# Optimization experiments

Hardware: AMD Instinct MI355X
Metric: run time of the kernel (lower is better)

Reference implementation:

```python
import jax, jax.numpy as jnp
import numpy as np

B, N, D, H = 2, 4096, 512, 8
HD = D // H

def setup_inputs() -> dict:
    key = jax.random.key(0)
    ks = jax.random.split(key, 5)
    s = 1.0 / np.sqrt(D)
    return {
        "x": jax.random.normal(ks[0], (B, N, D), dtype=jnp.float32),
        "W_qkv": jax.random.uniform(ks[1], (D, 3 * D), minval=-s, maxval=s, dtype=jnp.float32),
        "b_qkv": jax.random.uniform(ks[2], (3 * D,), minval=-s, maxval=s, dtype=jnp.float32),
        "W_out": jax.random.uniform(ks[3], (D, D), minval=-s, maxval=s, dtype=jnp.float32),
        "b_out": jax.random.uniform(ks[4], (D,), minval=-s, maxval=s, dtype=jnp.float32),
    }

def reference(x, W_qkv, b_qkv, W_out, b_out):
    Bq, Nq, Dq = x.shape
    scale = HD ** -0.5
    qkv = x @ W_qkv + b_qkv                      # [B,N,3D]
    qkv = qkv.reshape(Bq, Nq, 3, H, HD)
    q, k, v = (jnp.moveaxis(qkv[:, :, i], 2, 1) for i in range(3))  # [B,H,N,hd]
    attn = jnp.einsum('bhqd,bhkd->bhqk', q, k) * scale   # [B,H,N,N]
    causal = jnp.tril(jnp.ones((Nq, Nq), dtype=bool))
    attn = jnp.where(causal, attn, -jnp.inf)
    attn = jax.nn.softmax(attn, axis=-1)
    out = jnp.einsum('bhqk,bhkd->bhqd', attn, v)         # [B,H,N,hd]
    out = jnp.moveaxis(out, 1, 2).reshape(Bq, Nq, Dq)
    return out @ W_out + b_out
```

## Files before the change

kernel.cpp:

```cpp
#include <hip/hip_runtime.h>
#include <hip/hip_bf16.h>


typedef __bf16 bf16_t;
typedef __bf16 bf16x4 __attribute__((ext_vector_type(4)));
typedef __bf16 bf16x8 __attribute__((ext_vector_type(8)));
typedef float  f32x4  __attribute__((ext_vector_type(4)));


__global__ void convert_f32_bf16(const float* __restrict__ in, bf16_t* __restrict__ out) {
    int i = blockIdx.x * 256 + threadIdx.x;
    float4 v = ((const float4*)in)[i];
    bf16x4 o;
    o[0] = (bf16_t)v.x; o[1] = (bf16_t)v.y; o[2] = (bf16_t)v.z; o[3] = (bf16_t)v.w;
    ((bf16x4*)out)[i] = o;
}

__global__ void transpose_tiled(const float* __restrict__ in, bf16_t* __restrict__ out, int N) {
    __shared__ bf16_t T[64][72];
    const int tid = threadIdx.x;
    const int n0 = blockIdx.x * 64, k0 = blockIdx.y * 64;
    #pragma unroll
    for (int pass = 0; pass < 4; ++pass) {
        int kk = pass * 16 + (tid >> 4), nn = (tid & 15) * 4;
        float4 v = *(const float4*)(in + (size_t)(k0 + kk) * N + n0 + nn);
        T[nn + 0][kk] = (bf16_t)v.x; T[nn + 1][kk] = (bf16_t)v.y;
        T[nn + 2][kk] = (bf16_t)v.z; T[nn + 3][kk] = (bf16_t)v.w;
    }
    __syncthreads();
    #pragma unroll
    for (int pass = 0; pass < 2; ++pass) {
        int n = pass * 32 + (tid >> 3), c8 = (tid & 7) * 8;
        *(bf16x8*)(out + (size_t)(n0 + n) * 512 + k0 + c8) = *(const bf16x8*)&T[n][c8];
    }
}


template <int MODE, int TN>
__global__ __launch_bounds__(256) void gemm_bt(
    const bf16_t* __restrict__ A, const bf16_t* __restrict__ Bt,
    const float* __restrict__ bias,
    bf16_t* __restrict__ Qg, bf16_t* __restrict__ Kg, bf16_t* __restrict__ Vt,
    float* __restrict__ Cout)
{
    constexpr int NI = (TN == 128) ? 4 : 2;
    __shared__ bf16_t As[128][72];
    __shared__ bf16_t Bs[TN][72];
    const int tid  = threadIdx.x;
    const int wid  = tid >> 6, lane = tid & 63, l16 = lane & 15, quad = lane >> 4;
    const int wr   = (TN == 128) ? (wid >> 1) * 64 : wid * 32;
    const int wc   = (TN == 128) ? (wid & 1) * 64 : 0;
    const int m0   = blockIdx.y * 128, n0 = blockIdx.x * TN;

    f32x4 acc[NI][4] = {};

    for (int kk = 0; kk < 512; kk += 64) {
        __syncthreads();
        #pragma unroll
        for (int i = 0; i < 4; ++i) {
            int c = tid + i * 256, row = c >> 3, col8 = (c & 7) * 8;
            *(uint4*)&As[row][col8] = *(const uint4*)(A + (size_t)(m0 + row) * 512 + kk + col8);
        }
        #pragma unroll
        for (int i = 0; i < TN / 32; ++i) {
            int c = tid + i * 256, row = c >> 3, col8 = (c & 7) * 8;
            *(uint4*)&Bs[row][col8] = *(const uint4*)(Bt + (size_t)(n0 + row) * 512 + kk + col8);
        }
        __syncthreads();
        #pragma unroll
        for (int s = 0; s < 2; ++s) {
            bf16x8 a[NI], b[4];
            #pragma unroll
            for (int i = 0; i < NI; ++i) a[i] = *(const bf16x8*)&As[wr + i * 16 + l16][s * 32 + quad * 8];
            #pragma unroll
            for (int j = 0; j < 4; ++j) b[j] = *(const bf16x8*)&Bs[wc + j * 16 + l16][s * 32 + quad * 8];
            #pragma unroll
            for (int i = 0; i < NI; ++i)
                #pragma unroll
                for (int j = 0; j < 4; ++j)
                    acc[i][j] = __builtin_amdgcn_mfma_f32_16x16x32_bf16(a[i], b[j], acc[i][j], 0, 0, 0);
        }
    }

    const float qscale = 0.18033688011112042f;
    #pragma unroll
    for (int i = 0; i < NI; ++i) {
        int mrow = m0 + wr + i * 16 + quad * 4;
        #pragma unroll
        for (int j = 0; j < 4; ++j) {
            int cgl = n0 + wc + j * 16 + l16;
            float bv = bias[cgl];
            #pragma unroll
            for (int r = 0; r < 4; ++r) {
                int m = mrow + r;
                float val = acc[i][j][r] + bv;
                if (MODE == 0) {
                    int which = cgl >> 9, hh = (cgl >> 6) & 7, hd = cgl & 63;
                    int b_ = m >> 12, n = m & 4095, bh = b_ * 8 + hh;
                    if (which == 0)      Qg[((size_t)bh * 4096 + n) * 64 + hd] = (bf16_t)(val * qscale);
                    else if (which == 1) Kg[((size_t)bh * 4096 + n) * 64 + hd] = (bf16_t)val;
                    else                 Vt[((size_t)bh * 64 + hd) * 4096 + n] = (bf16_t)val;
                } else {
                    Cout[(size_t)m * 512 + cgl] = val;
                }
            }
        }
    }
}


__global__ __launch_bounds__(256, 3) void attn_ns2(
    const bf16_t* __restrict__ Qg, const bf16_t* __restrict__ Kg,
    const bf16_t* __restrict__ Vt,
    float* __restrict__ o_part, float* __restrict__ l_part, int nsplit)
{
    __shared__ bf16_t Ks[2][64][72];
    __shared__ bf16_t Vs[2][64][72];
    __shared__ bf16_t Ps[4][16][72];

    const int tid  = threadIdx.x;
    const int w    = tid >> 6, lane = tid & 63, l16 = lane & 15, quad = lane >> 4;
    const int bh   = blockIdx.x & 15, pr = (blockIdx.x >> 4) & 15, h = blockIdx.x >> 8;

    float* ob = o_part + (size_t)(h * 16 + bh) * 4096 * 64;
    float* lb = l_part + (size_t)(h * 16 + bh) * 4096;

    const int srow = tid >> 3, scol = (tid & 7) * 8;
    const int srow1 = srow + 32;
    const float MSHIFT = 12.0f;

    bf16x8 ones;
    #pragma unroll
    for (int j = 0; j < 8; ++j) ones[j] = (bf16_t)1.0f;

    uint4 kr0, kr1, vr0, vr1;

    for (int ph = 0; ph < 2; ++ph) {
        const int st = ph ? (31 - pr) : pr;
        const int T  = 2 * st + 2;
        const int b0 = (h * T) / nsplit, b1 = ((h + 1) * T) / nsplit;

        int qrow[2];
        bf16x8 qf[2][2];
        #pragma unroll
        for (int s = 0; s < 2; ++s) {
            qrow[s] = st * 128 + s * 64 + w * 16 + l16;
            const bf16_t* qp = Qg + ((size_t)bh * 4096 + qrow[s]) * 64;
            qf[s][0] = *(const bf16x8*)(qp + quad * 8);
            qf[s][1] = *(const bf16x8*)(qp + 32 + quad * 8);
        }

        f32x4 o[2][4] = {};
        f32x4 lacc[2] = {};

        {
            const size_t kb = ((size_t)bh * 4096 + b0 * 64) * 64;
            const size_t vb = (size_t)bh * 64 * 4096 + b0 * 64;
            kr0 = *(const uint4*)(Kg + kb + (size_t)srow * 64 + scol);
            kr1 = *(const uint4*)(Kg + kb + (size_t)srow1 * 64 + scol);
            vr0 = *(const uint4*)(Vt + vb + (size_t)srow * 4096 + scol);
            vr1 = *(const uint4*)(Vt + vb + (size_t)srow1 * 4096 + scol);
        }
        __syncthreads();

        for (int kt = b0; kt < b1; ++kt) {
            const int cur = kt & 1;
            *(uint4*)&Ks[cur][srow][scol]  = kr0;
            *(uint4*)&Ks[cur][srow1][scol] = kr1;
            *(uint4*)&Vs[cur][srow][scol]  = vr0;
            *(uint4*)&Vs[cur][srow1][scol] = vr1;
            __syncthreads();

            if (kt + 1 < b1) {
                const size_t kb = ((size_t)bh * 4096 + (kt + 1) * 64) * 64;
                const size_t vb = (size_t)bh * 64 * 4096 + (kt + 1) * 64;
                kr0 = *(const uint4*)(Kg + kb + (size_t)srow * 64 + scol);
                kr1 = *(const uint4*)(Kg + kb + (size_t)srow1 * 64 + scol);
                vr0 = *(const uint4*)(Vt + vb + (size_t)srow * 4096 + scol);
                vr1 = *(const uint4*)(Vt + vb + (size_t)srow1 * 4096 + scol);
            }

            bf16x8 kf[4][2], vf[4][2];
            #pragma unroll
            for (int cb = 0; cb < 4; ++cb) {
                kf[cb][0] = *(const bf16x8*)&Ks[cur][cb * 16 + l16][quad * 8];
                kf[cb][1] = *(const bf16x8*)&Ks[cur][cb * 16 + l16][32 + quad * 8];
            }
            #pragma unroll
            for (int j = 0; j < 4; ++j) {
                vf[j][0] = *(const bf16x8*)&Vs[cur][j * 16 + l16][quad * 8];
                vf[j][1] = *(const bf16x8*)&Vs[cur][j * 16 + l16][32 + quad * 8];
            }

            #pragma unroll
            for (int s = 0; s < 2; ++s) {
                const int diag = 2 * st + s;
                if (kt > diag) continue;

                f32x4 sv[4] = {};
                #pragma unroll
                for (int cb = 0; cb < 4; ++cb) {
                    sv[cb] = __builtin_amdgcn_mfma_f32_16x16x32_bf16(kf[cb][0], qf[s][0], sv[cb], 0, 0, 0);
                    sv[cb] = __builtin_amdgcn_mfma_f32_16x16x32_bf16(kf[cb][1], qf[s][1], sv[cb], 0, 0, 0);
                }

                if (kt == diag) {
                    #pragma unroll
                    for (int cb = 0; cb < 4; ++cb) {
                        const int keyg = kt * 64 + cb * 16 + quad * 4;
                        #pragma unroll
                        for (int r = 0; r < 4; ++r)
                            if (keyg + r > qrow[s]) sv[cb][r] = -1e30f;
                    }
                }

                #pragma unroll
                for (int cb = 0; cb < 4; ++cb) {
                    bf16x4 pk;
                    #pragma unroll
                    for (int r = 0; r < 4; ++r)
                        pk[r] = (bf16_t)__builtin_amdgcn_exp2f(sv[cb][r] - MSHIFT);
                    *(bf16x4*)&Ps[w][l16][cb * 16 + quad * 4] = pk;
                }
                bf16x8 pa0 = *(const bf16x8*)&Ps[w][l16][quad * 8];
                bf16x8 pa1 = *(const bf16x8*)&Ps[w][l16][32 + quad * 8];

                #pragma unroll
                for (int j = 0; j < 4; ++j) {
                    o[s][j] = __builtin_amdgcn_mfma_f32_16x16x32_bf16(pa0, vf[j][0], o[s][j], 0, 0, 0);
                    o[s][j] = __builtin_amdgcn_mfma_f32_16x16x32_bf16(pa1, vf[j][1], o[s][j], 0, 0, 0);
                }
                lacc[s] = __builtin_amdgcn_mfma_f32_16x16x32_bf16(pa0, ones, lacc[s], 0, 0, 0);
                lacc[s] = __builtin_amdgcn_mfma_f32_16x16x32_bf16(pa1, ones, lacc[s], 0, 0, 0);
            }
        }

        #pragma unroll
        for (int s = 0; s < 2; ++s)
            #pragma unroll
            for (int r = 0; r < 4; ++r) {
                int n = st * 128 + s * 64 + w * 16 + quad * 4 + r;
                #pragma unroll
                for (int j = 0; j < 4; ++j)
                    ob[(size_t)n * 64 + j * 16 + l16] = o[s][j][r];
                if (l16 == 0) lb[n] = lacc[s][r];
            }
    }
}

__global__ void combine_kernel(const float* __restrict__ o_part,
                               const float* __restrict__ l_part,
                               bf16_t* __restrict__ Og, int ns)
{
    int t = blockIdx.x * 256 + threadIdx.x;
    int oct = t & 7, n = (t >> 3) & 4095, bh = t >> 15;
    size_t base = ((size_t)bh * 4096 + n) * 64 + oct * 8;
    f32x4 s0 = {}, s1 = {};
    float l = 0.f;
    for (int h = 0; h < ns; ++h) {
        const float* op = o_part + (size_t)h * 16 * 4096 * 64 + base;
        s0 += *(const f32x4*)op;
        s1 += *(const f32x4*)(op + 4);
        l  += l_part[(size_t)h * 16 * 4096 + (size_t)bh * 4096 + n];
    }
    float inv = 1.0f / l;
    bf16x8 res;
    #pragma unroll
    for (int j = 0; j < 4; ++j) {
        res[j]     = (bf16_t)(s0[j] * inv);
        res[j + 4] = (bf16_t)(s1[j] * inv);
    }
    *(bf16x8*)(Og + ((size_t)((bh >> 3) * 4096 + n)) * 512 + (bh & 7) * 64 + oct * 8) = res;
}


extern "C" void kernel_launch(void* const* d_in, const int* in_sizes, int n_in,
                              void* d_out, int out_size, void* d_ws, size_t ws_size,
                              hipStream_t stream) {
    const float* x    = (const float*)d_in[0];
    const float* Wqkv = (const float*)d_in[1];
    const float* bqkv = (const float*)d_in[2];
    const float* Wout = (const float*)d_in[3];
    const float* bout = (const float*)d_in[4];
    float* out = (float*)d_out;

    char* ws = (char*)d_ws;
    bf16_t* xb  = (bf16_t*)(ws);
    bf16_t* WqT = (bf16_t*)(ws + 8388608);
    bf16_t* WoT = (bf16_t*)(ws + 9961472);
    bf16_t* Qg  = (bf16_t*)(ws + 10485760);
    bf16_t* Kg  = (bf16_t*)(ws + 18874368);
    bf16_t* Vt  = (bf16_t*)(ws + 27262976);

    const int nsplit = (ws_size >= 86769664ULL) ? 3 : 2;
    float* o_part = (float*)(ws + 35651584);
    float* l_part = (float*)(ws + 35651584 + (size_t)nsplit * 16777216);

    convert_f32_bf16<<<4096, 256, 0, stream>>>(x, xb);
    transpose_tiled<<<dim3(24, 8), 256, 0, stream>>>(Wqkv, WqT, 1536);
    transpose_tiled<<<dim3(8, 8), 256, 0, stream>>>(Wout, WoT, 512);

    gemm_bt<0, 128><<<dim3(12, 64), 256, 0, stream>>>(xb, WqT, bqkv, Qg, Kg, Vt, nullptr);

    attn_ns2<<<256 * nsplit, 256, 0, stream>>>(Qg, Kg, Vt, o_part, l_part, nsplit);
    combine_kernel<<<2048, 256, 0, stream>>>(o_part, l_part, xb , nsplit);

    gemm_bt<1, 64><<<dim3(8, 64), 256, 0, stream>>>(xb, WoT, bout, nullptr, nullptr, nullptr, out);
}
```

Baseline: 200.7 us.

## Load GEMM tiles directly to LDS with XOR swizzle; split V transpose out

The GEMM tile loads now go through global_load_lds (16-byte direct-to-LDS), and an XOR-swizzled unpadded layout replaces the padded LDS arrays to avoid bank conflicts without register staging. The QKV epilogue previously wrote V transposed with strided scattered stores. It now writes V row-major into a scratch region that aliases o_part, and a separate swizzled LDS transpose kernel produces Vt. This adds one kernel launch and an extra pass over V in exchange for coalesced epilogue stores and cheaper GEMM loads.

```diff
diff --git a/kernel.cpp b/kernel.cpp
--- a/kernel.cpp
+++ b/kernel.cpp
@@ -6,6 +6,12 @@
 typedef __bf16 bf16x4 __attribute__((ext_vector_type(4)));
 typedef __bf16 bf16x8 __attribute__((ext_vector_type(8)));
 typedef float  f32x4  __attribute__((ext_vector_type(4)));
+
+__device__ __forceinline__ void gload_lds16(const bf16_t* g, bf16_t* l) {
+    __builtin_amdgcn_global_load_lds(
+        (const __attribute__((address_space(1))) void*)g,
+        (__attribute__((address_space(3))) void*)l, 16, 0, 0);
+}
 
 
 __global__ void convert_f32_bf16(const float* __restrict__ in, bf16_t* __restrict__ out) {
@@ -35,19 +41,44 @@
     }
 }
 
+__global__ void transpose_v(const bf16_t* __restrict__ Vg, bf16_t* __restrict__ Vt) {
+    __shared__ bf16_t T[64 * 64];
+    const int tid = threadIdx.x;
+    const int bh = blockIdx.x >> 6, n0 = (blockIdx.x & 63) * 64;
+    const bf16_t* src = Vg + ((size_t)bh * 4096 + n0) * 64;
+    #pragma unroll
+    for (int i = 0; i < 2; ++i) {
+        int c = tid + i * 256, n = c >> 3, h8 = (c & 7) * 8;
+        bf16x8 v = *(const bf16x8*)(src + (size_t)n * 64 + h8);
+        const int swz = (n >> 3) ^ (h8 >> 3);
+        bf16_t* base = &T[swz * 8 + (n & 7)];
+        #pragma unroll
+        for (int j = 0; j < 8; ++j) base[(h8 + j) * 64] = v[j];
+    }
+    __syncthreads();
+    bf16_t* dst = Vt + (size_t)bh * 64 * 4096 + n0;
+    #pragma unroll
+    for (int i = 0; i < 2; ++i) {
+        int c = tid + i * 256, hd = c >> 3, cn = c & 7;
+        *(bf16x8*)(dst + (size_t)hd * 4096 + cn * 8) =
+            *(const bf16x8*)&T[hd * 64 + ((cn ^ (hd >> 3)) * 8)];
+    }
+}
+
 
 template <int MODE, int TN>
 __global__ __launch_bounds__(256) void gemm_bt(
     const bf16_t* __restrict__ A, const bf16_t* __restrict__ Bt,
     const float* __restrict__ bias,
-    bf16_t* __restrict__ Qg, bf16_t* __restrict__ Kg, bf16_t* __restrict__ Vt,
+    bf16_t* __restrict__ Qg, bf16_t* __restrict__ Kg, bf16_t* __restrict__ Vg,
     float* __restrict__ Cout)
 {
     constexpr int NI = (TN == 128) ? 4 : 2;
-    __shared__ bf16_t As[128][72];
-    __shared__ bf16_t Bs[TN][72];
+    __shared__ bf16_t As[128 * 64];
+    __shared__ bf16_t Bs[TN * 64];
     const int tid  = threadIdx.x;
     const int wid  = tid >> 6, lane = tid & 63, l16 = lane & 15, quad = lane >> 4;
+    const int l8   = l16 & 7;
     const int wr   = (TN == 128) ? (wid >> 1) * 64 : wid * 32;
     const int wc   = (TN == 128) ? (wid & 1) * 64 : 0;
     const int m0   = blockIdx.y * 128, n0 = blockIdx.x * TN;
@@ -58,22 +89,33 @@
         __syncthreads();
         #pragma unroll
         for (int i = 0; i < 4; ++i) {
-            int c = tid + i * 256, row = c >> 3, col8 = (c & 7) * 8;
-            *(uint4*)&As[row][col8] = *(const uint4*)(A + (size_t)(m0 + row) * 512 + kk + col8);
+            int slot = tid + i * 256;
+            int row = slot >> 3, cg = (slot & 7) ^ (row & 7);
+            gload_lds16(A + (size_t)(m0 + row) * 512 + kk + cg * 8,
+                        (bf16_t*)((char*)As + ((i * 256 + (wid << 6)) << 4)));
         }
         #pragma unroll
         for (int i = 0; i < TN / 32; ++i) {
-            int c = tid + i * 256, row = c >> 3, col8 = (c & 7) * 8;
-            *(uint4*)&Bs[row][col8] = *(const uint4*)(Bt + (size_t)(n0 + row) * 512 + kk + col8);
+            int slot = tid + i * 256;
+            int row = slot >> 3, cg = (slot & 7) ^ (row & 7);
+            gload_lds16(Bt + (size_t)(n0 + row) * 512 + kk + cg * 8,
+                        (bf16_t*)((char*)Bs + ((i * 256 + (wid << 6)) << 4)));
         }
         __syncthreads();
         #pragma unroll
         for (int s = 0; s < 2; ++s) {
+            const int sw = (s * 4 + quad);
             bf16x8 a[NI], b[4];
             #pragma unroll
-            for (int i = 0; i < NI; ++i) a[i] = *(const bf16x8*)&As[wr + i * 16 + l16][s * 32 + quad * 8];
-            #pragma unroll
-            for (int j = 0; j < 4; ++j) b[j] = *(const bf16x8*)&Bs[wc + j * 16 + l16][s * 32 + quad * 8];
+            for (int i = 0; i < NI; ++i) {
+                int row = wr + i * 16 + l16;
+                a[i] = *(const bf16x8*)&As[(row * 8 + (sw ^ l8)) * 8];
+            }
+            #pragma unroll
+            for (int j = 0; j < 4; ++j) {
+                int row = wc + j * 16 + l16;
+                b[j] = *(const bf16x8*)&Bs[(row * 8 + (sw ^ l8)) * 8];
+            }
             #pragma unroll
             for (int i = 0; i < NI; ++i)
                 #pragma unroll
@@ -97,9 +139,10 @@
                 if (MODE == 0) {
                     int which = cgl >> 9, hh = (cgl >> 6) & 7, hd = cgl & 63;
                     int b_ = m >> 12, n = m & 4095, bh = b_ * 8 + hh;
-                    if (which == 0)      Qg[((size_t)bh * 4096 + n) * 64 + hd] = (bf16_t)(val * qscale);
-                    else if (which == 1) Kg[((size_t)bh * 4096 + n) * 64 + hd] = (bf16_t)val;
-                    else                 Vt[((size_t)bh * 64 + hd) * 4096 + n] = (bf16_t)val;
+                    size_t idx = ((size_t)bh * 4096 + n) * 64 + hd;
+                    if (which == 0)      Qg[idx] = (bf16_t)(val * qscale);
+                    else if (which == 1) Kg[idx] = (bf16_t)val;
+                    else                 Vg[idx] = (bf16_t)val;
                 } else {
                     Cout[(size_t)m * 512 + cgl] = val;
                 }
@@ -291,6 +334,7 @@
     bf16_t* Qg  = (bf16_t*)(ws + 10485760);
     bf16_t* Kg  = (bf16_t*)(ws + 18874368);
     bf16_t* Vt  = (bf16_t*)(ws + 27262976);
+    bf16_t* Vg  = (bf16_t*)(ws + 35651584);
 
     const int nsplit = (ws_size >= 86769664ULL) ? 3 : 2;
     float* o_part = (float*)(ws + 35651584);
@@ -300,7 +344,8 @@
     transpose_tiled<<<dim3(24, 8), 256, 0, stream>>>(Wqkv, WqT, 1536);
     transpose_tiled<<<dim3(8, 8), 256, 0, stream>>>(Wout, WoT, 512);
 
-    gemm_bt<0, 128><<<dim3(12, 64), 256, 0, stream>>>(xb, WqT, bqkv, Qg, Kg, Vt, nullptr);
+    gemm_bt<0, 128><<<dim3(12, 64), 256, 0, stream>>>(xb, WqT, bqkv, Qg, Kg, Vg, nullptr);
+    transpose_v<<<1024, 256, 0, stream>>>(Vg, Vt);
 
     attn_ns2<<<256 * nsplit, 256, 0, stream>>>(Qg, Kg, Vt, o_part, l_part, nsplit);
     combine_kernel<<<2048, 256, 0, stream>>>(o_part, l_part, xb , nsplit);
```

Result: faster. 191.0 us (-4.8%).
